# Performance work log

Hardware: AMD Instinct MI355X
Metric: run time of the kernel (lower is better)

The kernel has to match this reference:

```python
import jax, jax.numpy as jnp
import numpy as np

B = 256          # batch
MID = 16384      # mid_siz
OUT = 16384      # out_siz
C = 16           # channel_siz
NLVL = 8         # nlvl (== klvl here since floor(log2(OUT/2))=13 >= 8)
MIDF = MID >> NLVL   # mid_filter_siz = 64
OUTF = OUT >> NLVL   # out_filter_siz = 64
NB = 1 << NLVL       # 256 leaf branches
STD = 0.5


def setup_inputs() -> dict:
    key = jax.random.key(0)
    ks = jax.random.split(key, 6)
    in_data = jax.random.normal(ks[0], (B, MID, 2), jnp.float32)
    # learned parameters (buildRand: normal(0, 0.5) filters, zero biases)
    mid_dense = jax.random.normal(ks[1], (1, MID, 2), jnp.float32) * STD
    in_filter = jax.random.normal(ks[2], (MIDF, 1, C), jnp.float32) * STD   # conv1d [width,in,out]
    in_bias = jnp.zeros((C,), jnp.float32)
    # level lvl (1..NLVL) uses filters[lvl-1, :2**lvl]; padded to NB branches
    filters = jax.random.normal(ks[3], (NLVL, NB, 2, C, C), jnp.float32) * STD
    biases = jnp.zeros((NLVL, NB, C), jnp.float32)
    fea_dense = jax.random.normal(ks[4], (NB, C, OUTF), jnp.float32) * STD
    return dict(in_data=in_data, mid_dense=mid_dense, in_filter=in_filter,
                in_bias=in_bias, filters=filters, biases=biases, fea_dense=fea_dense)


def reference(in_data, mid_dense, in_filter, in_bias, filters, biases, fea_dense):
    # elementwise modulation then split real/imag channels: (B, 2, MID)
    x = jnp.moveaxis(in_data * mid_dense, -1, 1)
    # level-0 conv1d: kernel MIDF, stride MIDF//2 -> overlapping half-windows.
    # Split signal into half-width chunks h; window t = [h[t], h[t+1]].
    half = MIDF // 2
    h = x.reshape(B, 2, MID // half, half)                 # (B,2,512,32)
    W1 = in_filter[:half, 0, :]                            # (32,C)
    W2 = in_filter[half:, 0, :]
    s = jnp.einsum('bisw,wc->bisc', h[:, :, :-1], W1) \
        + jnp.einsum('bisw,wc->bisc', h[:, :, 1:], W2)
    s = jax.nn.relu(s + in_bias)                           # (B,2,2^(n+1)-1,C)
    state = s[:, :, None]                                  # (B,2,nb=1,L,C)
    # butterfly tree: each level doubles branches; conv kernel=2, stride=2, VALID
    for lvl in range(1, NLVL + 1):
        nb = 1 << lvl
        p = jnp.repeat(state, 2, axis=2)                   # child itk <- parent itk//2
        L = p.shape[3]                                     # odd: 2^(n+1-lvl+1)-1
        xw = p[:, :, :, :L - 1, :].reshape(B, 2, nb, (L - 1) // 2, 2, C)
        W = filters[lvl - 1, :nb]                          # (nb,2,C,C)
        bb = biases[lvl - 1, :nb]                          # (nb,C)
        state = jax.nn.relu(
            jnp.einsum('bintkc,nkcd->bintd', xw, W) + bb[None, None, :, None, :])
    feat = state[:, :, :, 0, :]                            # (B,2,NB,C): L==1 at last level
    outp = jnp.einsum('binc,ncf->binf', feat, fea_dense)   # per-branch dense projection
    R = outp[:, 0].reshape(B, OUT // 2, 2)
    I = outp[:, 1].reshape(B, OUT // 2, 2)
    out_data = ((R[:, :, 0] - I[:, :, 1]) / MID).reshape(B, OUT // 2, 1)
    return out_data, R[:, :, 1]
```

## Files before the change

### kernel.cpp

```cpp
#include <hip/hip_runtime.h>
#include <hip/hip_bf16.h>


#define OUT_HALF 2097152

typedef __attribute__((ext_vector_type(4))) float f32x4;
typedef __attribute__((ext_vector_type(8))) short s16x8;

__device__ __forceinline__ uint fsw(uint a) {
    return a ^ ((((a >> 6) ^ (a >> 8)) & 3u) << 4);
}
__device__ __forceinline__ ushort bfr(float f) {
    __hip_bfloat16 h = __float2bfloat16(f);
    union { __hip_bfloat16 h; ushort u; } cv; cv.h = h; return cv.u;
}
__device__ __forceinline__ uint pk(float a, float b) {
    return (uint)bfr(a) | ((uint)bfr(b) << 16);
}

__device__ __forceinline__ void tree_level(
    char* smb, const int lane, const int wave,
    uint AOff, uint NOff, int lgR, int lgNP, int nTiles,
    uint WOff, int wnb, uint LBOff, int bnb)
{
    const int m  = lane & 15;
    const int kg = lane >> 4;
    const int lgTPP = lgR - 4;
    for (int at = wave; at < nTiles; at += 4) {
        const int p  = at >> lgTPP;
        const int tc = at & ((1 << lgTPP) - 1);
        const int np = p & ((1 << lgNP) - 1);
        const int ii = p >> lgNP;
        s16x8 af = *(const s16x8*)(smb + AOff + (p << (lgR + 6)) +
                                   fsw((uint)((tc * 16 + m) * 64 + kg * 16)));
#pragma unroll
        for (int sib = 0; sib < 2; sib++) {
            const int nl = 2 * np + sib;
            s16x8 bf = *(const s16x8*)(smb + WOff +
                         fsw((uint)((wnb + nl) * 1024 + m * 64 + kg * 16)));
            float bv = *(const float*)(smb + LBOff + ((bnb + nl) * 16 + m) * 4);
            f32x4 acc = {bv, bv, bv, bv};
            acc = __builtin_amdgcn_mfma_f32_16x16x32_bf16(af, bf, acc, 0, 0, 0);
            const int p2 = (ii << (lgNP + 1)) + nl;
            const uint wb = NOff + (p2 << (lgR + 5));
            const int r2 = tc * 8 + kg * 2;
            *(uint*)(smb + wb + fsw((uint)(r2 * 64 + m * 4))) =
                pk(fmaxf(acc.x, 0.f), fmaxf(acc.y, 0.f));
            *(uint*)(smb + wb + fsw((uint)((r2 + 1) * 64 + m * 4))) =
                pk(fmaxf(acc.z, 0.f), fmaxf(acc.w, 0.f));
        }
    }
}

__global__ __launch_bounds__(256, 4)
void ibf_A(const float* __restrict__ in_data, const float* __restrict__ mid_dense,
           const float* __restrict__ in_filter, const float* __restrict__ in_bias,
           const float* __restrict__ filters, const float* __restrict__ biases,
           uint* __restrict__ S3)
{
    __shared__ __align__(16) char smb[29760];
    const int tid = threadIdx.x, lane = tid & 63, wave = tid >> 6;
    const int b = blockIdx.x;
    const int th = blockIdx.y >> 1;
    const int i  = blockIdx.y & 1;

    {
        const float4* inb = (const float4*)in_data + (size_t)b * 8192 + th * 2048;
        const float4* mdb = (const float4*)mid_dense + th * 2048;
        for (int mp = tid; mp < 2064; mp += 256) {
            float4 iv = inb[mp], mv = mdb[mp];
            float xa = i ? iv.y * mv.y : iv.x * mv.x;
            float xb = i ? iv.w * mv.w : iv.z * mv.z;
            *(uint*)(smb + fsw((uint)(mp * 4))) = pk(xa, xb);
        }
    }
    for (int t = tid; t < 3584; t += 256) {
        int nidx = t >> 8, r = t & 255, d = r & 15, c = r >> 4;
        int lvl = (nidx < 2) ? 1 : ((nidx < 6) ? 2 : 3);
        int n = nidx - ((1 << lvl) - 2);
        const float* src = filters + (size_t)(lvl - 1) * 131072 + n * 512 + c * 16 + d;
        *(uint*)(smb + 12416 + fsw((uint)(nidx * 1024 + d * 64 + c * 4))) = pk(src[0], src[256]);
    }
    for (int t = tid; t < 512; t += 256) {
        int c = t >> 5, w2 = t & 31;
        *(uint*)(smb + 26752 + fsw((uint)(c * 128 + w2 * 4))) =
            pk(in_filter[(2 * w2) * 16 + c], in_filter[(2 * w2 + 1) * 16 + c]);
    }
    if (tid < 240) {
        float v;
        if (tid < 224) {
            int nidx = tid >> 4;
            int lvl = (nidx < 2) ? 1 : ((nidx < 6) ? 2 : 3);
            int n = nidx - ((1 << lvl) - 2);
            v = biases[(size_t)(lvl - 1) * 4096 + n * 16 + (tid & 15)];
        } else v = in_bias[tid - 224];
        *(float*)(smb + 28800 + tid * 4) = v;
    }
    __syncthreads();

    {
        const int m = lane & 15, kg = lane >> 4;
        s16x8 b0 = *(const s16x8*)(smb + 26752 + fsw((uint)(m * 128 + kg * 16)));
        s16x8 b1 = *(const s16x8*)(smb + 26752 + fsw((uint)(m * 128 + 64 + kg * 16)));
        float bv = *(const float*)(smb + 28800 + (224 + m) * 4);
        for (int at = wave; at < 8; at += 4) {
            int tc = at;
            s16x8 a0 = *(const s16x8*)(smb + fsw((uint)((tc * 16 + m) * 64 + kg * 16)));
            s16x8 a1 = *(const s16x8*)(smb + fsw((uint)((tc * 16 + m) * 64 + 64 + kg * 16)));
            f32x4 acc = {bv, bv, bv, bv};
            acc = __builtin_amdgcn_mfma_f32_16x16x32_bf16(a0, b0, acc, 0, 0, 0);
            acc = __builtin_amdgcn_mfma_f32_16x16x32_bf16(a1, b1, acc, 0, 0, 0);
            int r2 = tc * 8 + kg * 2;
            *(uint*)(smb + 8320 + fsw((uint)(r2 * 64 + m * 4))) =
                pk(fmaxf(acc.x, 0.f), fmaxf(acc.y, 0.f));
            *(uint*)(smb + 8320 + fsw((uint)((r2 + 1) * 64 + m * 4))) =
                pk(fmaxf(acc.z, 0.f), fmaxf(acc.w, 0.f));
        }
    }
    __syncthreads();
    tree_level(smb, lane, wave, 8320, 0,    6, 0, 4, 12416, 0, 28800, 0);
    __syncthreads();
    tree_level(smb, lane, wave, 0,    8320, 5, 1, 4, 12416, 2, 28800, 2);
    __syncthreads();
    {
        const int m = lane & 15, kg = lane >> 4;
        for (int at = wave; at < 4; at += 4) {
            s16x8 af = *(const s16x8*)(smb + 8320 + (at << 10) + fsw((uint)(m * 64 + kg * 16)));
#pragma unroll
            for (int sib = 0; sib < 2; sib++) {
                int n3 = 2 * at + sib;
                s16x8 bf = *(const s16x8*)(smb + 12416 +
                             fsw((uint)((6 + n3) * 1024 + m * 64 + kg * 16)));
                float bv = *(const float*)(smb + 28800 + ((6 + n3) * 16 + m) * 4);
                f32x4 acc = {bv, bv, bv, bv};
                acc = __builtin_amdgcn_mfma_f32_16x16x32_bf16(af, bf, acc, 0, 0, 0);
                int bi = 2 * b + i;
                int t4 = th * 8 + kg * 2;
                uint idx = ((uint)(n3 * 512 + bi) * 16 + t4) * 16 + m;
                S3[idx]      = pk(fmaxf(acc.x, 0.f), fmaxf(acc.y, 0.f));
                S3[idx + 16] = pk(fmaxf(acc.z, 0.f), fmaxf(acc.w, 0.f));
            }
        }
    }
}

__global__ __launch_bounds__(256, 2)
void ibf_B(const float* __restrict__ filters, const float* __restrict__ biases,
           const uint* __restrict__ S3, char* __restrict__ S8)
{
    __shared__ __align__(16) char smb[61312];
    const int tid = threadIdx.x, lane = tid & 63, wave = tid >> 6;
    const int n3 = blockIdx.x, chunk = blockIdx.y;

    {
        const char* src = (const char*)S3 + ((size_t)n3 * 512 + chunk * 8) * 1024;
        for (int ci = tid; ci < 512; ci += 256)
            *(float4*)(smb + fsw((uint)(ci * 16))) = *(const float4*)(src + ci * 16);
    }
    for (int t = tid; t < 992; t += 256) {
        int nidx = t >> 4, q = nidx + 2;
        int l3 = 31 - __clz(q);
        int nl = q - (1 << l3);
        int gn = (n3 << l3) + nl;
        *(float*)(smb + 57344 + t * 4) = biases[(size_t)(l3 + 2) * 4096 + gn * 16 + (t & 15)];
    }
    auto stage_w = [&](int l3) {
        int NL = 1 << l3;
        const float* fb = filters + (size_t)(l3 + 2) * 131072;
        for (int t = tid; t < NL * 256; t += 256) {
            int nl = t >> 8, r = t & 255, d = r & 15, c = r >> 4;
            const float* src = fb + (size_t)((n3 << l3) + nl) * 512 + c * 16 + d;
            *(uint*)(smb + 24576 + fsw((uint)(nl * 1024 + d * 64 + c * 4))) = pk(src[0], src[256]);
        }
    };
    stage_w(1);
    __syncthreads();
    tree_level(smb, lane, wave, 0,    8192, 7, 0, 8, 24576, 0, 57344, 0);
    __syncthreads();
    stage_w(2);
    __syncthreads();
    tree_level(smb, lane, wave, 8192, 0,    6, 1, 8, 24576, 0, 57344, 2);
    __syncthreads();
    stage_w(3);
    __syncthreads();
    tree_level(smb, lane, wave, 0,    8192, 5, 2, 8, 24576, 0, 57344, 6);
    __syncthreads();
    stage_w(4);
    __syncthreads();
    tree_level(smb, lane, wave, 8192, 0,    4, 3, 8, 24576, 0, 57344, 14);
    __syncthreads();
    stage_w(5);
    __syncthreads();
    {
        const int m = lane & 15, kg = lane >> 4;
        for (int at = wave; at < 16; at += 4) {
            s16x8 af = *(const s16x8*)(smb + at * 512 + fsw((uint)(m * 64 + kg * 16)));
#pragma unroll
            for (int sib = 0; sib < 2; sib++) {
                int nl = 2 * at + sib;
                s16x8 bf = *(const s16x8*)(smb + 24576 +
                             fsw((uint)(nl * 1024 + m * 64 + kg * 16)));
                float bv = *(const float*)(smb + 57344 + ((30 + nl) * 16 + m) * 4);
                f32x4 acc = {bv, bv, bv, bv};
                acc = __builtin_amdgcn_mfma_f32_16x16x32_bf16(af, bf, acc, 0, 0, 0);
                if (kg < 2) {
                    float v[4] = {fmaxf(acc.x, 0.f), fmaxf(acc.y, 0.f),
                                  fmaxf(acc.z, 0.f), fmaxf(acc.w, 0.f)};
#pragma unroll
                    for (int j = 0; j < 4; j++)
                        *(ushort*)(smb + 16384 + nl * 256 + (kg * 4 + j) * 32 + m * 2) = bfr(v[j]);
                }
            }
        }
    }
    __syncthreads();
    {
        float4* dst = (float4*)(S8 + (size_t)(n3 * 64 + chunk) * 8192);
        for (int ci = tid; ci < 512; ci += 256)
            dst[ci] = *(const float4*)(smb + 16384 + ci * 16);
    }
}

__global__ __launch_bounds__(256, 4)
void ibf_C(const float* __restrict__ fea_dense, const char* __restrict__ S8,
           float* __restrict__ out)
{
    __shared__ ushort FEb[1024];
    const int tid = threadIdx.x, lane = tid & 63, wave = tid >> 6;
    const int n8g = blockIdx.x, q = blockIdx.y;
    const int n3 = n8g >> 5, n8l = n8g & 31;

    for (int idx = tid; idx < 1024; idx += 256) {
        int c = idx >> 6, u = idx & 63;
        FEb[u * 16 + c] = bfr(fea_dense[(size_t)n8g * 1024 + idx]);
    }
    __syncthreads();

    const int m = lane & 15, kg = lane >> 4;
    s16x8 bfrg[4];
#pragma unroll
    for (int ut = 0; ut < 4; ut++) {
        if (kg < 2) bfrg[ut] = *(const s16x8*)(FEb + (ut * 16 + m) * 16 + kg * 8);
        else        bfrg[ut] = (s16x8){0, 0, 0, 0, 0, 0, 0, 0};
    }
    for (int w = 0; w < 2; w++) {
        const int tile  = q * 8 + wave * 2 + w;
        const int birow = tile * 16 + m;
        s16x8 af = {0, 0, 0, 0, 0, 0, 0, 0};
        if (kg < 2)
            af = *(const s16x8*)(S8 + ((size_t)(n3 * 64 + (birow >> 3)) * 32 + n8l) * 256
                                 + (birow & 7) * 32 + kg * 16);
        const int b0  = (tile * 16 + kg * 4) >> 1;
        const bool odd = (m & 1);
#pragma unroll
        for (int ut = 0; ut < 4; ut++) {
            f32x4 acc = {0.f, 0.f, 0.f, 0.f};
            acc = __builtin_amdgcn_mfma_f32_16x16x32_bf16(af, bfrg[ut], acc, 0, 0, 0);
            float sy = __shfl_xor(acc.y, 1);
            float sw = __shfl_xor(acc.w, 1);
            const int g = n8g * 32 + ut * 8 + (m >> 1);
            float v0 = odd ? acc.x : (acc.x - sy) * (1.f / 16384.f);
            float v1 = odd ? acc.z : (acc.z - sw) * (1.f / 16384.f);
            size_t off = (odd ? (size_t)OUT_HALF : (size_t)0) + (size_t)g;
            out[(size_t)b0 * 8192 + off]       = v0;
            out[(size_t)(b0 + 1) * 8192 + off] = v1;
        }
    }
}

extern "C" void kernel_launch(void* const* d_in, const int* in_sizes, int n_in,
                              void* d_out, int out_size, void* d_ws, size_t ws_size,
                              hipStream_t stream) {
    const float* in_data   = (const float*)d_in[0];
    const float* mid_dense = (const float*)d_in[1];
    const float* in_filter = (const float*)d_in[2];
    const float* in_bias   = (const float*)d_in[3];
    const float* filters   = (const float*)d_in[4];
    const float* biases    = (const float*)d_in[5];
    const float* fea_dense = (const float*)d_in[6];
    float* out = (float*)d_out;
    uint* S3   = (uint*)d_ws;
    char* S8   = (char*)d_ws + (4 << 20);

    ibf_A<<<dim3(256, 4), 256, 0, stream>>>(in_data, mid_dense, in_filter, in_bias,
                                            filters, biases, S3);
    ibf_B<<<dim3(8, 64), 256, 0, stream>>>(filters, biases, S3, S8);
    ibf_C<<<dim3(256, 4), 256, 0, stream>>>(fea_dense, S8, out);
}
```

Measured before the change: 41.16 us.

## Fuse tree levels and dense projection into single-wave kernels with register weights

Replaces the three-kernel pipeline with two kernels. Both use single-wave 64-thread blocks, keep filter fragments in registers loaded straight from global memory, and need no block-level barriers. The later tree levels and the final fea_dense projection are fused into one kernel, which drops the S8 workspace round trip and one launch. The risks are that fea_dense and filters are reloaded and converted to bf16 redundantly in every block, and that small blocks issue many uncoalesced scalar global loads.

New measurement: 50.27 us. +22.1%, slower.

```diff
diff --git a/kernel.cpp b/kernel.cpp
--- a/kernel.cpp
+++ b/kernel.cpp
@@ -6,6 +6,8 @@
 
 typedef __attribute__((ext_vector_type(4))) float f32x4;
 typedef __attribute__((ext_vector_type(8))) short s16x8;
+
+extern __shared__ char smb[];
 
 __device__ __forceinline__ uint fsw(uint a) {
     return a ^ ((((a >> 6) ^ (a >> 8)) & 3u) << 4);
@@ -18,125 +20,113 @@
     return (uint)bfr(a) | ((uint)bfr(b) << 16);
 }
 
-__device__ __forceinline__ void tree_level(
-    char* smb, const int lane, const int wave,
-    uint AOff, uint NOff, int lgR, int lgNP, int nTiles,
-    uint WOff, int wnb, uint LBOff, int bnb)
-{
-    const int m  = lane & 15;
-    const int kg = lane >> 4;
-    const int lgTPP = lgR - 4;
-    for (int at = wave; at < nTiles; at += 4) {
-        const int p  = at >> lgTPP;
-        const int tc = at & ((1 << lgTPP) - 1);
-        const int np = p & ((1 << lgNP) - 1);
-        const int ii = p >> lgNP;
-        s16x8 af = *(const s16x8*)(smb + AOff + (p << (lgR + 6)) +
-                                   fsw((uint)((tc * 16 + m) * 64 + kg * 16)));
-#pragma unroll
-        for (int sib = 0; sib < 2; sib++) {
-            const int nl = 2 * np + sib;
-            s16x8 bf = *(const s16x8*)(smb + WOff +
-                         fsw((uint)((wnb + nl) * 1024 + m * 64 + kg * 16)));
-            float bv = *(const float*)(smb + LBOff + ((bnb + nl) * 16 + m) * 4);
-            f32x4 acc = {bv, bv, bv, bv};
-            acc = __builtin_amdgcn_mfma_f32_16x16x32_bf16(af, bf, acc, 0, 0, 0);
-            const int p2 = (ii << (lgNP + 1)) + nl;
-            const uint wb = NOff + (p2 << (lgR + 5));
-            const int r2 = tc * 8 + kg * 2;
-            *(uint*)(smb + wb + fsw((uint)(r2 * 64 + m * 4))) =
-                pk(fmaxf(acc.x, 0.f), fmaxf(acc.y, 0.f));
-            *(uint*)(smb + wb + fsw((uint)((r2 + 1) * 64 + m * 4))) =
-                pk(fmaxf(acc.z, 0.f), fmaxf(acc.w, 0.f));
-        }
-    }
-}
-
-__global__ __launch_bounds__(256, 4)
+#define LDFRAG(dst, fb)                                                      \
+    {                                                                        \
+        const float* s_ = (fb) + m;                                          \
+        _Pragma("unroll")                                                    \
+        for (int cq_ = 0; cq_ < 4; cq_++) {                                  \
+            int c_ = kg * 4 + cq_;                                           \
+            (&(dst).x)[cq_] = pk(s_[c_ * 16], s_[256 + c_ * 16]);            \
+        }                                                                    \
+    }
+#define PACKW(baseoff, r2)                                                              \
+    *(uint*)(smb + fsw((uint)((baseoff) + (r2) * 64 + m * 4))) =                        \
+        pk(fmaxf(acc.x, 0.f), fmaxf(acc.y, 0.f));                                       \
+    *(uint*)(smb + fsw((uint)((baseoff) + ((r2) + 1) * 64 + m * 4))) =                  \
+        pk(fmaxf(acc.z, 0.f), fmaxf(acc.w, 0.f));
+
+__global__ __launch_bounds__(64, 2)
 void ibf_A(const float* __restrict__ in_data, const float* __restrict__ mid_dense,
            const float* __restrict__ in_filter, const float* __restrict__ in_bias,
            const float* __restrict__ filters, const float* __restrict__ biases,
            uint* __restrict__ S3)
 {
-    __shared__ __align__(16) char smb[29760];
-    const int tid = threadIdx.x, lane = tid & 63, wave = tid >> 6;
+    const int lane = threadIdx.x;
+    const int m = lane & 15, kg = lane >> 4;
     const int b = blockIdx.x;
-    const int th = blockIdx.y >> 1;
-    const int i  = blockIdx.y & 1;
+    const int i = blockIdx.y >> 2;
+    const int w = blockIdx.y & 3;
 
     {
-        const float4* inb = (const float4*)in_data + (size_t)b * 8192 + th * 2048;
-        const float4* mdb = (const float4*)mid_dense + th * 2048;
-        for (int mp = tid; mp < 2064; mp += 256) {
-            float4 iv = inb[mp], mv = mdb[mp];
+        const float4* inb = (const float4*)in_data + (size_t)b * 8192 + (size_t)w * 1024;
+        const float4* mdb = (const float4*)mid_dense + (size_t)w * 1024;
+        for (int ip = lane; ip < 1040; ip += 64) {
+            float4 iv = inb[ip], mv = mdb[ip];
             float xa = i ? iv.y * mv.y : iv.x * mv.x;
             float xb = i ? iv.w * mv.w : iv.z * mv.z;
-            *(uint*)(smb + fsw((uint)(mp * 4))) = pk(xa, xb);
-        }
-    }
-    for (int t = tid; t < 3584; t += 256) {
-        int nidx = t >> 8, r = t & 255, d = r & 15, c = r >> 4;
-        int lvl = (nidx < 2) ? 1 : ((nidx < 6) ? 2 : 3);
-        int n = nidx - ((1 << lvl) - 2);
-        const float* src = filters + (size_t)(lvl - 1) * 131072 + n * 512 + c * 16 + d;
-        *(uint*)(smb + 12416 + fsw((uint)(nidx * 1024 + d * 64 + c * 4))) = pk(src[0], src[256]);
-    }
-    for (int t = tid; t < 512; t += 256) {
-        int c = t >> 5, w2 = t & 31;
-        *(uint*)(smb + 26752 + fsw((uint)(c * 128 + w2 * 4))) =
-            pk(in_filter[(2 * w2) * 16 + c], in_filter[(2 * w2 + 1) * 16 + c]);
-    }
-    if (tid < 240) {
-        float v;
-        if (tid < 224) {
-            int nidx = tid >> 4;
-            int lvl = (nidx < 2) ? 1 : ((nidx < 6) ? 2 : 3);
-            int n = nidx - ((1 << lvl) - 2);
-            v = biases[(size_t)(lvl - 1) * 4096 + n * 16 + (tid & 15)];
-        } else v = in_bias[tid - 224];
-        *(float*)(smb + 28800 + tid * 4) = v;
-    }
-    __syncthreads();
-
-    {
-        const int m = lane & 15, kg = lane >> 4;
-        s16x8 b0 = *(const s16x8*)(smb + 26752 + fsw((uint)(m * 128 + kg * 16)));
-        s16x8 b1 = *(const s16x8*)(smb + 26752 + fsw((uint)(m * 128 + 64 + kg * 16)));
-        float bv = *(const float*)(smb + 28800 + (224 + m) * 4);
-        for (int at = wave; at < 8; at += 4) {
-            int tc = at;
-            s16x8 a0 = *(const s16x8*)(smb + fsw((uint)((tc * 16 + m) * 64 + kg * 16)));
-            s16x8 a1 = *(const s16x8*)(smb + fsw((uint)((tc * 16 + m) * 64 + 64 + kg * 16)));
-            f32x4 acc = {bv, bv, bv, bv};
-            acc = __builtin_amdgcn_mfma_f32_16x16x32_bf16(a0, b0, acc, 0, 0, 0);
-            acc = __builtin_amdgcn_mfma_f32_16x16x32_bf16(a1, b1, acc, 0, 0, 0);
-            int r2 = tc * 8 + kg * 2;
-            *(uint*)(smb + 8320 + fsw((uint)(r2 * 64 + m * 4))) =
-                pk(fmaxf(acc.x, 0.f), fmaxf(acc.y, 0.f));
-            *(uint*)(smb + 8320 + fsw((uint)((r2 + 1) * 64 + m * 4))) =
-                pk(fmaxf(acc.z, 0.f), fmaxf(acc.w, 0.f));
-        }
-    }
-    __syncthreads();
-    tree_level(smb, lane, wave, 8320, 0,    6, 0, 4, 12416, 0, 28800, 0);
-    __syncthreads();
-    tree_level(smb, lane, wave, 0,    8320, 5, 1, 4, 12416, 2, 28800, 2);
-    __syncthreads();
-    {
-        const int m = lane & 15, kg = lane >> 4;
-        for (int at = wave; at < 4; at += 4) {
-            s16x8 af = *(const s16x8*)(smb + 8320 + (at << 10) + fsw((uint)(m * 64 + kg * 16)));
-#pragma unroll
-            for (int sib = 0; sib < 2; sib++) {
-                int n3 = 2 * at + sib;
-                s16x8 bf = *(const s16x8*)(smb + 12416 +
-                             fsw((uint)((6 + n3) * 1024 + m * 64 + kg * 16)));
-                float bv = *(const float*)(smb + 28800 + ((6 + n3) * 16 + m) * 4);
-                f32x4 acc = {bv, bv, bv, bv};
-                acc = __builtin_amdgcn_mfma_f32_16x16x32_bf16(af, bf, acc, 0, 0, 0);
-                int bi = 2 * b + i;
-                int t4 = th * 8 + kg * 2;
-                uint idx = ((uint)(n3 * 512 + bi) * 16 + t4) * 16 + m;
+            *(uint*)(smb + fsw((uint)(ip * 4))) = pk(xa, xb);
+        }
+    }
+    s16x8 b0f, b1f;
+#pragma unroll
+    for (int j = 0; j < 8; j++) {
+        b0f[j] = (short)bfr(in_filter[(kg * 8 + j) * 16 + m]);
+        b1f[j] = (short)bfr(in_filter[(32 + kg * 8 + j) * 16 + m]);
+    }
+    float bv0 = in_bias[m];
+    uint4 w1[2]; float bv1[2];
+#pragma unroll
+    for (int n = 0; n < 2; n++) {
+        LDFRAG(w1[n], filters + (size_t)n * 512);
+        bv1[n] = biases[n * 16 + m];
+    }
+    uint4 w2[4]; float bv2[4];
+#pragma unroll
+    for (int n = 0; n < 4; n++) {
+        LDFRAG(w2[n], filters + 131072 + (size_t)n * 512);
+        bv2[n] = biases[4096 + n * 16 + m];
+    }
+    uint4 w3[8]; float bv3[8];
+#pragma unroll
+    for (int n = 0; n < 8; n++) {
+        LDFRAG(w3[n], filters + 2 * 131072 + (size_t)n * 512);
+        bv3[n] = biases[2 * 4096 + n * 16 + m];
+    }
+
+#pragma unroll
+    for (int tc = 0; tc < 4; tc++) {
+        s16x8 a0 = *(const s16x8*)(smb + fsw((uint)((tc * 16 + m) * 64 + kg * 16)));
+        s16x8 a1 = *(const s16x8*)(smb + fsw((uint)((tc * 16 + m) * 64 + 64 + kg * 16)));
+        f32x4 acc = {bv0, bv0, bv0, bv0};
+        acc = __builtin_amdgcn_mfma_f32_16x16x32_bf16(a0, b0f, acc, 0, 0, 0);
+        acc = __builtin_amdgcn_mfma_f32_16x16x32_bf16(a1, b1f, acc, 0, 0, 0);
+        const int r2 = tc * 8 + kg * 2;
+        PACKW(4224, r2);
+    }
+#pragma unroll
+    for (int tc = 0; tc < 2; tc++) {
+        s16x8 af = *(const s16x8*)(smb + fsw((uint)(4224 + (tc * 16 + m) * 64 + kg * 16)));
+#pragma unroll
+        for (int s = 0; s < 2; s++) {
+            f32x4 acc = {bv1[s], bv1[s], bv1[s], bv1[s]};
+            acc = __builtin_amdgcn_mfma_f32_16x16x32_bf16(af, *(const s16x8*)&w1[s], acc, 0, 0, 0);
+            const int r2 = tc * 8 + kg * 2;
+            PACKW(6272 + s * 1024, r2);
+        }
+    }
+#pragma unroll
+    for (int p = 0; p < 2; p++) {
+        s16x8 af = *(const s16x8*)(smb + fsw((uint)(6272 + p * 1024 + m * 64 + kg * 16)));
+#pragma unroll
+        for (int s = 0; s < 2; s++) {
+            const int nl = 2 * p + s;
+            f32x4 acc = {bv2[nl], bv2[nl], bv2[nl], bv2[nl]};
+            acc = __builtin_amdgcn_mfma_f32_16x16x32_bf16(af, *(const s16x8*)&w2[nl], acc, 0, 0, 0);
+            const int r2 = kg * 2;
+            PACKW(8320 + nl * 512, r2);
+        }
+    }
+    const int bi = 2 * b + i;
+#pragma unroll
+    for (int p = 0; p < 4; p++) {
+        s16x8 af = *(const s16x8*)(smb + fsw((uint)(8320 + p * 512 + m * 64 + kg * 16)));
+#pragma unroll
+        for (int s = 0; s < 2; s++) {
+            const int nl = 2 * p + s;
+            f32x4 acc = {bv3[nl], bv3[nl], bv3[nl], bv3[nl]};
+            acc = __builtin_amdgcn_mfma_f32_16x16x32_bf16(af, *(const s16x8*)&w3[nl], acc, 0, 0, 0);
+            if (kg < 2) {
+                const uint idx = ((uint)(nl * 512 + bi) * 16 + (uint)(4 * w + kg * 2)) * 16 + m;
                 S3[idx]      = pk(fmaxf(acc.x, 0.f), fmaxf(acc.y, 0.f));
                 S3[idx + 16] = pk(fmaxf(acc.z, 0.f), fmaxf(acc.w, 0.f));
             }
@@ -144,126 +134,133 @@
     }
 }
 
-__global__ __launch_bounds__(256, 2)
-void ibf_B(const float* __restrict__ filters, const float* __restrict__ biases,
-           const uint* __restrict__ S3, char* __restrict__ S8)
+__global__ __launch_bounds__(64, 2)
+void ibf_BC(const float* __restrict__ filters, const float* __restrict__ biases,
+            const float* __restrict__ fea_dense, const uint* __restrict__ S3,
+            float* __restrict__ out)
 {
-    __shared__ __align__(16) char smb[61312];
-    const int tid = threadIdx.x, lane = tid & 63, wave = tid >> 6;
-    const int n3 = blockIdx.x, chunk = blockIdx.y;
-
-    {
-        const char* src = (const char*)S3 + ((size_t)n3 * 512 + chunk * 8) * 1024;
-        for (int ci = tid; ci < 512; ci += 256)
-            *(float4*)(smb + fsw((uint)(ci * 16))) = *(const float4*)(src + ci * 16);
-    }
-    for (int t = tid; t < 992; t += 256) {
-        int nidx = t >> 4, q = nidx + 2;
-        int l3 = 31 - __clz(q);
-        int nl = q - (1 << l3);
-        int gn = (n3 << l3) + nl;
-        *(float*)(smb + 57344 + t * 4) = biases[(size_t)(l3 + 2) * 4096 + gn * 16 + (t & 15)];
-    }
-    auto stage_w = [&](int l3) {
-        int NL = 1 << l3;
-        const float* fb = filters + (size_t)(l3 + 2) * 131072;
-        for (int t = tid; t < NL * 256; t += 256) {
-            int nl = t >> 8, r = t & 255, d = r & 15, c = r >> 4;
-            const float* src = fb + (size_t)((n3 << l3) + nl) * 512 + c * 16 + d;
-            *(uint*)(smb + 24576 + fsw((uint)(nl * 1024 + d * 64 + c * 4))) = pk(src[0], src[256]);
-        }
-    };
-    stage_w(1);
-    __syncthreads();
-    tree_level(smb, lane, wave, 0,    8192, 7, 0, 8, 24576, 0, 57344, 0);
-    __syncthreads();
-    stage_w(2);
-    __syncthreads();
-    tree_level(smb, lane, wave, 8192, 0,    6, 1, 8, 24576, 0, 57344, 2);
-    __syncthreads();
-    stage_w(3);
-    __syncthreads();
-    tree_level(smb, lane, wave, 0,    8192, 5, 2, 8, 24576, 0, 57344, 6);
-    __syncthreads();
-    stage_w(4);
-    __syncthreads();
-    tree_level(smb, lane, wave, 8192, 0,    4, 3, 8, 24576, 0, 57344, 14);
-    __syncthreads();
-    stage_w(5);
-    __syncthreads();
-    {
-        const int m = lane & 15, kg = lane >> 4;
-        for (int at = wave; at < 16; at += 4) {
-            s16x8 af = *(const s16x8*)(smb + at * 512 + fsw((uint)(m * 64 + kg * 16)));
-#pragma unroll
-            for (int sib = 0; sib < 2; sib++) {
-                int nl = 2 * at + sib;
-                s16x8 bf = *(const s16x8*)(smb + 24576 +
-                             fsw((uint)(nl * 1024 + m * 64 + kg * 16)));
-                float bv = *(const float*)(smb + 57344 + ((30 + nl) * 16 + m) * 4);
-                f32x4 acc = {bv, bv, bv, bv};
-                acc = __builtin_amdgcn_mfma_f32_16x16x32_bf16(af, bf, acc, 0, 0, 0);
-                if (kg < 2) {
-                    float v[4] = {fmaxf(acc.x, 0.f), fmaxf(acc.y, 0.f),
-                                  fmaxf(acc.z, 0.f), fmaxf(acc.w, 0.f)};
-#pragma unroll
-                    for (int j = 0; j < 4; j++)
-                        *(ushort*)(smb + 16384 + nl * 256 + (kg * 4 + j) * 32 + m * 2) = bfr(v[j]);
-                }
-            }
-        }
-    }
-    __syncthreads();
-    {
-        float4* dst = (float4*)(S8 + (size_t)(n3 * 64 + chunk) * 8192);
-        for (int ci = tid; ci < 512; ci += 256)
-            dst[ci] = *(const float4*)(smb + 16384 + ci * 16);
-    }
-}
-
-__global__ __launch_bounds__(256, 4)
-void ibf_C(const float* __restrict__ fea_dense, const char* __restrict__ S8,
-           float* __restrict__ out)
-{
-    __shared__ ushort FEb[1024];
-    const int tid = threadIdx.x, lane = tid & 63, wave = tid >> 6;
-    const int n8g = blockIdx.x, q = blockIdx.y;
-    const int n3 = n8g >> 5, n8l = n8g & 31;
-
-    for (int idx = tid; idx < 1024; idx += 256) {
-        int c = idx >> 6, u = idx & 63;
-        FEb[u * 16 + c] = bfr(fea_dense[(size_t)n8g * 1024 + idx]);
-    }
-    __syncthreads();
-
+    const int lane = threadIdx.x;
     const int m = lane & 15, kg = lane >> 4;
-    s16x8 bfrg[4];
-#pragma unroll
-    for (int ut = 0; ut < 4; ut++) {
-        if (kg < 2) bfrg[ut] = *(const s16x8*)(FEb + (ut * 16 + m) * 16 + kg * 8);
-        else        bfrg[ut] = (s16x8){0, 0, 0, 0, 0, 0, 0, 0};
-    }
-    for (int w = 0; w < 2; w++) {
-        const int tile  = q * 8 + wave * 2 + w;
-        const int birow = tile * 16 + m;
-        s16x8 af = {0, 0, 0, 0, 0, 0, 0, 0};
-        if (kg < 2)
-            af = *(const s16x8*)(S8 + ((size_t)(n3 * 64 + (birow >> 3)) * 32 + n8l) * 256
-                                 + (birow & 7) * 32 + kg * 16);
-        const int b0  = (tile * 16 + kg * 4) >> 1;
-        const bool odd = (m & 1);
+    const int n3 = blockIdx.x;
+    const int c4 = blockIdx.y >> 1;
+    const int n4 = 2 * n3 + (blockIdx.y & 1);
+    const int bi0 = c4 * 4;
+
+    uint4 f4; float bv4;
+    LDFRAG(f4, filters + 3 * 131072 + (size_t)n4 * 512);
+    bv4 = biases[3 * 4096 + n4 * 16 + m];
+    uint4 f5[2]; float bv5[2];
+#pragma unroll
+    for (int n = 0; n < 2; n++) {
+        LDFRAG(f5[n], filters + 4 * 131072 + (size_t)(2 * n4 + n) * 512);
+        bv5[n] = biases[4 * 4096 + (2 * n4 + n) * 16 + m];
+    }
+    uint4 f6[4]; float bv6[4];
+#pragma unroll
+    for (int n = 0; n < 4; n++) {
+        LDFRAG(f6[n], filters + 5 * 131072 + (size_t)(4 * n4 + n) * 512);
+        bv6[n] = biases[5 * 4096 + (4 * n4 + n) * 16 + m];
+    }
+    uint4 f7[8]; float bv7[8];
+#pragma unroll
+    for (int n = 0; n < 8; n++) {
+        LDFRAG(f7[n], filters + 6 * 131072 + (size_t)(8 * n4 + n) * 512);
+        bv7[n] = biases[6 * 4096 + (8 * n4 + n) * 16 + m];
+    }
+
+#pragma unroll
+    for (int tc = 0; tc < 4; tc++) {
+        const char* rb = (const char*)S3 + (size_t)(n3 * 512 + bi0 + tc) * 1024;
+        s16x8 af = *(const s16x8*)(rb + m * 64 + kg * 16);
+        f32x4 acc = {bv4, bv4, bv4, bv4};
+        acc = __builtin_amdgcn_mfma_f32_16x16x32_bf16(af, *(const s16x8*)&f4, acc, 0, 0, 0);
+        const int r2 = tc * 8 + kg * 2;
+        PACKW(0, r2);
+    }
+#pragma unroll
+    for (int tc = 0; tc < 2; tc++) {
+        s16x8 af = *(const s16x8*)(smb + fsw((uint)((tc * 16 + m) * 64 + kg * 16)));
+#pragma unroll
+        for (int s = 0; s < 2; s++) {
+            f32x4 acc = {bv5[s], bv5[s], bv5[s], bv5[s]};
+            acc = __builtin_amdgcn_mfma_f32_16x16x32_bf16(af, *(const s16x8*)&f5[s], acc, 0, 0, 0);
+            const int r2 = tc * 8 + kg * 2;
+            PACKW(2048 + s * 1024, r2);
+        }
+    }
+#pragma unroll
+    for (int p = 0; p < 2; p++) {
+        s16x8 af = *(const s16x8*)(smb + fsw((uint)(2048 + p * 1024 + m * 64 + kg * 16)));
+#pragma unroll
+        for (int s = 0; s < 2; s++) {
+            const int nl = 2 * p + s;
+            f32x4 acc = {bv6[nl], bv6[nl], bv6[nl], bv6[nl]};
+            acc = __builtin_amdgcn_mfma_f32_16x16x32_bf16(af, *(const s16x8*)&f6[nl], acc, 0, 0, 0);
+            const int r2 = kg * 2;
+            PACKW(4096 + nl * 512, r2);
+        }
+    }
+#pragma unroll
+    for (int p = 0; p < 4; p++) {
+        s16x8 af = *(const s16x8*)(smb + fsw((uint)(4096 + p * 512 + m * 64 + kg * 16)));
+#pragma unroll
+        for (int s = 0; s < 2; s++) {
+            const int nl = 2 * p + s;
+            f32x4 acc = {bv7[nl], bv7[nl], bv7[nl], bv7[nl]};
+            acc = __builtin_amdgcn_mfma_f32_16x16x32_bf16(af, *(const s16x8*)&f7[nl], acc, 0, 0, 0);
+            if (kg < 2) {
+                const int r2 = kg * 2;
+                PACKW(6144 + nl * 256, r2);
+            }
+        }
+    }
+#pragma unroll
+    for (int p = 0; p < 8; p++) {
+        s16x8 af = *(const s16x8*)(smb + fsw((uint)(6144 + p * 256 + m * 64 + kg * 16)));
+#pragma unroll
+        for (int s = 0; s < 2; s++) {
+            const int nl = 2 * p + s;
+            uint4 f8; LDFRAG(f8, filters + 7 * 131072 + (size_t)(16 * n4 + nl) * 512);
+            float bv8 = biases[7 * 4096 + (16 * n4 + nl) * 16 + m];
+            f32x4 acc = {bv8, bv8, bv8, bv8};
+            acc = __builtin_amdgcn_mfma_f32_16x16x32_bf16(af, *(const s16x8*)&f8, acc, 0, 0, 0);
+            if (kg == 0) {
+                float v[4] = {fmaxf(acc.x, 0.f), fmaxf(acc.y, 0.f),
+                              fmaxf(acc.z, 0.f), fmaxf(acc.w, 0.f)};
+#pragma unroll
+                for (int j = 0; j < 4; j++)
+                    *(ushort*)(smb + 8192 + nl * 512 + j * 32 + m * 2) = bfr(v[j]);
+            }
+        }
+    }
+    const float inv = 1.f / 16384.f;
+    const float* feb = fea_dense + (size_t)(n4 * 16) * 1024;
+#pragma unroll 2
+    for (int nl8 = 0; nl8 < 16; nl8++) {
+        s16x8 bf = {0, 0, 0, 0, 0, 0, 0, 0};
+        if (kg < 2) bf = *(const s16x8*)(smb + 8192 + nl8 * 512 + m * 32 + kg * 16);
+        const float* fp = feb + nl8 * 1024;
+        const int gj0 = (n4 * 16 + nl8) * 32;
 #pragma unroll
         for (int ut = 0; ut < 4; ut++) {
+            s16x8 af = {0, 0, 0, 0, 0, 0, 0, 0};
+            if (kg < 2) {
+                const float* fa = fp + (kg * 8) * 64 + ut * 16 + m;
+#pragma unroll
+                for (int j = 0; j < 8; j++) af[j] = (short)bfr(fa[j * 64]);
+            }
             f32x4 acc = {0.f, 0.f, 0.f, 0.f};
-            acc = __builtin_amdgcn_mfma_f32_16x16x32_bf16(af, bfrg[ut], acc, 0, 0, 0);
+            acc = __builtin_amdgcn_mfma_f32_16x16x32_bf16(af, bf, acc, 0, 0, 0);
             float sy = __shfl_xor(acc.y, 1);
             float sw = __shfl_xor(acc.w, 1);
-            const int g = n8g * 32 + ut * 8 + (m >> 1);
-            float v0 = odd ? acc.x : (acc.x - sy) * (1.f / 16384.f);
-            float v1 = odd ? acc.z : (acc.z - sw) * (1.f / 16384.f);
-            size_t off = (odd ? (size_t)OUT_HALF : (size_t)0) + (size_t)g;
-            out[(size_t)b0 * 8192 + off]       = v0;
-            out[(size_t)(b0 + 1) * 8192 + off] = v1;
+            if (((m & 1) == 0) && m < 4) {
+                const int b0 = 2 * c4 + (m >> 1);
+                const int j = gj0 + ut * 8 + kg * 2;
+                *(float2*)(out + (size_t)b0 * 8192 + j) =
+                    make_float2((acc.x - sy) * inv, (acc.z - sw) * inv);
+                *(float2*)(out + OUT_HALF + (size_t)b0 * 8192 + j) =
+                    make_float2(acc.y, acc.w);
+            }
         }
     }
 }
@@ -280,10 +277,8 @@
     const float* fea_dense = (const float*)d_in[6];
     float* out = (float*)d_out;
     uint* S3   = (uint*)d_ws;
-    char* S8   = (char*)d_ws + (4 << 20);
-
-    ibf_A<<<dim3(256, 4), 256, 0, stream>>>(in_data, mid_dense, in_filter, in_bias,
-                                            filters, biases, S3);
-    ibf_B<<<dim3(8, 64), 256, 0, stream>>>(filters, biases, S3, S8);
-    ibf_C<<<dim3(256, 4), 256, 0, stream>>>(fea_dense, S8, out);
-}
+
+    ibf_A<<<dim3(256, 8), 64, 11392, stream>>>(in_data, mid_dense, in_filter, in_bias,
+                                               filters, biases, S3);
+    ibf_BC<<<dim3(8, 256), 64, 16384, stream>>>(filters, biases, fea_dense, S3, out);
+}
```
